# Optimization experiments

Hardware: AMD Instinct MI355X
Metric: run time of the kernel (lower is better)

The kernel has to match this reference:

```python
import jax, jax.numpy as jnp
import numpy as np

SELF_DIM = 36
ENT_DIM = 28
HID = 256


def setup_inputs() -> dict:
    key = jax.random.key(0)
    ks = jax.random.split(key, 12)
    B, agent_num, n_noisy = 32768, 20, 20
    obs_dim = SELF_DIM + ENT_DIM * (2 * agent_num - 1 + n_noisy)
    s = 0.02
    return {
        "x": jax.random.normal(ks[0], (B, obs_dim), dtype=jnp.float32),
        "Watt": jax.random.normal(ks[1], (ENT_DIM + SELF_DIM, 1), jnp.float32) * s,
        "batt": jnp.zeros((1,), jnp.float32),
        "We": jax.random.normal(ks[2], (ENT_DIM + SELF_DIM, HID), jnp.float32) * s,
        "be": jnp.zeros((HID,), jnp.float32),
        "Wse": jax.random.normal(ks[3], (2 * SELF_DIM, HID), jnp.float32) * s,
        "bse": jnp.zeros((HID,), jnp.float32),
        "Wg": jax.random.normal(ks[4], (3 * HID, 3), jnp.float32) * s,
        "bg": jnp.zeros((3,), jnp.float32),
        "Wo": jax.random.normal(ks[5], (2 * HID, HID), jnp.float32) * s,
        "bo": jnp.zeros((HID,), jnp.float32),
        "agent_num": agent_num,
    }


def reference(x, Watt, batt, We, be, Wse, bse, Wg, bg, Wo, bo, agent_num):
    B = x.shape[0]
    self_info = x[:, :SELF_DIM]  # [B,36]
    opp_end = SELF_DIM + ENT_DIM * agent_num
    par_end = opp_end + ENT_DIM * (agent_num - 1)
    opps = x[:, SELF_DIM:opp_end].reshape(B, agent_num, ENT_DIM)
    pars = x[:, opp_end:par_end].reshape(B, agent_num - 1, ENT_DIM)
    noisy = x[:, par_end:].reshape(B, -1, ENT_DIM)

    def pool(ent):
        # additive-attention pooling over one entity group
        n = ent.shape[1]
        os_ = jnp.concatenate(
            [jnp.broadcast_to(self_info[:, None, :], (B, n, SELF_DIM)), ent], axis=2
        )  # [B,n,64]
        att = jax.nn.softmax(os_ @ Watt + batt, axis=1)  # [B,n,1]
        es = os_ @ We + be  # [B,n,H]
        return jnp.sum(att * es, axis=1)  # [B,H]

    opp_e, par_e, noi_e = pool(opps), pool(pars), pool(noisy)
    group_e = jnp.stack([opp_e, par_e, noi_e], axis=1)  # [B,3,H]
    gw = jax.nn.softmax(
        jnp.concatenate([opp_e, par_e, noi_e], axis=1) @ Wg + bg, axis=1
    )  # [B,3]
    other = jnp.einsum("bg,bgh->bh", gw, group_e)  # [B,H]
    self_e = jnp.concatenate([self_info, self_info], axis=1) @ Wse + bse  # [B,H]
    obs_embedding = jnp.concatenate([other, self_e], axis=1)  # [B,2H]
    return obs_embedding @ Wo + bo
```

## Files before the change

kernel.cpp:

```cpp
#include <hip/hip_runtime.h>
#include <hip/hip_bf16.h>

#define SELF_D 36
#define ENT_D  28
#define HID    256
#define OBS    1688
#define NWAVES 8192

#define WS_A     0
#define WS_B     9216
#define WS_C     16384
#define WS_MSEL  16640
#define WS_MENT  16748
#define WS_CG    17000
#define WS_WATT  17008
#define WS_AT    17040
#define WS_BT    26256
#define WS_TOTAL 33424

__global__ __launch_bounds__(256)
void setup_kernel(const float* __restrict__ Watt, const float* __restrict__ We,
                  const float* __restrict__ be,  const float* __restrict__ Wse,
                  const float* __restrict__ bse, const float* __restrict__ Wg,
                  const float* __restrict__ bg,  const float* __restrict__ Wo,
                  const float* __restrict__ bo,  float* __restrict__ ws) {
  const int blk = blockIdx.x;
  const int c = threadIdx.x;
  if (blk < 36) {
    int k = blk;
    float acc = 0.f;
    for (int r = 0; r < 256; ++r) acc += We[k*256 + r] * Wo[r*256 + c];
    for (int r = 0; r < 256; ++r) acc += (Wse[k*256 + r] + Wse[(36+k)*256 + r]) * Wo[(256+r)*256 + c];
    ws[WS_A + k*256 + c] = acc;
    ws[WS_AT + c*36 + k] = acc;
  } else if (blk < 64) {
    int k = blk - 36;
    float acc = 0.f;
    for (int r = 0; r < 256; ++r) acc += We[(36+k)*256 + r] * Wo[r*256 + c];
    ws[WS_B + k*256 + c] = acc;
    ws[WS_BT + c*28 + k] = acc;
  } else if (blk == 64) {
    float acc = bo[c];
    for (int r = 0; r < 256; ++r) acc += be[r] * Wo[r*256 + c];
    for (int r = 0; r < 256; ++r) acc += bse[r] * Wo[(256+r)*256 + c];
    ws[WS_C + c] = acc;
  } else {
    for (int t = c; t < 391; t += 256) {
      if (t < 108) {
        int k = t / 3, j = t - 3*k;
        float acc = 0.f;
        for (int r = 0; r < 256; ++r) {
          float wg = Wg[r*3 + j] + Wg[(256+r)*3 + j] + Wg[(512+r)*3 + j];
          acc += We[k*256 + r] * wg;
        }
        ws[WS_MSEL + t] = acc;
      } else if (t < 360) {
        int idx = t - 108;
        int g = idx / 84, rem = idx - 84*g;
        int k = rem / 3, j = rem - 3*k;
        float acc = 0.f;
        for (int r = 0; r < 256; ++r) acc += We[(36+k)*256 + r] * Wg[(256*g + r)*3 + j];
        ws[WS_MENT + idx] = acc;
      } else if (t < 363) {
        int j = t - 360;
        float acc = bg[j];
        for (int r = 0; r < 256; ++r)
          acc += be[r] * (Wg[r*3 + j] + Wg[(256+r)*3 + j] + Wg[(512+r)*3 + j]);
        ws[WS_CG + j] = acc;
      } else {
        int k = t - 363;
        ws[WS_WATT + k] = Watt[36 + k];
      }
    }
  }
}

__global__ __launch_bounds__(256)
void pool_kernel(const float* __restrict__ x, const float* __restrict__ ws,
                 float* __restrict__ out, int B) {
  __shared__ __align__(16) float tile[4][OBS];
  __shared__ __align__(16) float satt[4][64];
  __shared__ __align__(16) float sebar[4][84];
  __shared__ __align__(16) float sW[28];
  __shared__ __align__(16) float sM[360];

  const int tid = threadIdx.x;
  const int w = tid >> 6, ln = tid & 63;

  for (int t = tid; t < 360; t += 256) sM[t] = ws[WS_MSEL + t];
  if (tid < 28) sW[tid] = ws[WS_WATT + tid];
  __syncthreads();

  const float cg0 = ws[WS_CG + 0], cg1 = ws[WS_CG + 1], cg2 = ws[WS_CG + 2];

  const int ent_b  = ln - (ln >= 40 ? 1 : 0);
  const bool valid = (ln < 60) && (ln != 39);
  const int ent_r  = valid ? ent_b : 0;
  int e7 = ent_r;
  while (e7 >= 7) e7 -= 7;
  const int gj = ln >> 4, gch = ln & 15;
  const bool gact = (gj < 3) && (gch < 15);

  for (int row = blockIdx.x * 4 + w; row < B; row += NWAVES) {
    const float* xr = x + (size_t)row * OBS;

#pragma unroll
    for (int i = 0; i < 7; ++i) {
      int idx = i * 64 + ln;
      if (idx < OBS / 4) {
        __builtin_amdgcn_global_load_lds(
            (const __attribute__((address_space(1))) void*)(xr + idx * 4),
            (__attribute__((address_space(3))) void*)(&tile[w][0] + idx * 4),
            16, 0, 0);
      }
    }
    asm volatile("s_waitcnt vmcnt(0)" ::: "memory");
    __builtin_amdgcn_sched_barrier(0);

    float l = -1e30f;
    {
      const float4* ep = (const float4*)&tile[w][SELF_D + ENT_D * ent_r];
      const float4* w4 = (const float4*)sW;
      float acc = 0.f;
#pragma unroll
      for (int t = 0; t < 7; ++t) {
        int c = e7 + t; if (c >= 7) c -= 7;
        float4 v = ep[c], wv = w4[c];
        acc += v.x*wv.x + v.y*wv.y + v.z*wv.z + v.w*wv.w;
      }
      if (valid) l = acc;
    }
    float m = l;
#pragma unroll
    for (int off = 32; off; off >>= 1) m = fmaxf(m, __shfl_xor(m, off));
    satt[w][ln] = valid ? __expf(l - m) : 0.f;

#pragma unroll
    for (int pass = 0; pass < 2; ++pass) {
      int t = ln + pass * 64;
      if (t < 84) {
        int g = t / 28, k = t - 28 * g;
        int e0 = g * 20 - (g >> 1);
        const float* vb = &tile[w][SELF_D + ENT_D * e0 + k];
        const float* pa = &satt[w][g * 20];
        float us = 0.f, uv = 0.f;
#pragma unroll
        for (int i = 0; i < 20; ++i) {
          float pp = pa[i];
          float vv = vb[ENT_D * i];
          us += pp; uv += pp * vv;
        }
        sebar[w][t] = uv / us;
      }
    }

    float gl = 0.f;
    if (gact) {
#pragma unroll
      for (int q = 0; q < 8; ++q) {
        int c = q * 15 + gch;
        float v = (c < SELF_D) ? tile[w][c] : sebar[w][c - SELF_D];
        gl += v * sM[c * 3 + gj];
      }
    }
#pragma unroll
    for (int off = 1; off < 16; off <<= 1) gl += __shfl_xor(gl, off);
    float l0 = __shfl(gl, 0)  + cg0;
    float l1 = __shfl(gl, 16) + cg1;
    float l2 = __shfl(gl, 32) + cg2;
    float mm = fmaxf(l0, fmaxf(l1, l2));
    float e0x = __expf(l0 - mm), e1x = __expf(l1 - mm), e2x = __expf(l2 - mm);
    float inv = 1.f / (e0x + e1x + e2x);

    float fv;
    if (ln < SELF_D) {
      fv = tile[w][ln];
    } else {
      int k = ln - SELF_D;
      fv = (e0x * sebar[w][k] + e1x * sebar[w][28 + k] + e2x * sebar[w][56 + k]) * inv;
    }
    out[(size_t)row * HID + ln] = fv;
  }
}

#define PR_ROWS 32
#define PR_CH   8
__global__ __launch_bounds__(256)
void proj_kernel(const float* __restrict__ ws, float* __restrict__ out) {
  __shared__ __align__(16) float sf[PR_CH][64];
  const int tid = threadIdx.x;

  float4 Av[9], Bv[7];
#pragma unroll
  for (int q = 0; q < 9; ++q) Av[q] = ((const float4*)(ws + WS_AT + tid * 36))[q];
#pragma unroll
  for (int q = 0; q < 7; ++q) Bv[q] = ((const float4*)(ws + WS_BT + tid * 28))[q];
  const float cc = ws[WS_C + tid];

  const size_t row0 = (size_t)blockIdx.x * PR_ROWS;
  for (int chk = 0; chk < PR_ROWS / PR_CH; ++chk) {
    const size_t rbase = row0 + chk * PR_CH;
    if (tid < PR_CH * 16) {
      int r = tid >> 4, q = tid & 15;
      ((float4*)&sf[r][0])[q] = ((const float4*)(out + (rbase + r) * HID))[q];
    }
    __syncthreads();
#pragma unroll
    for (int r = 0; r < PR_CH; ++r) {
      float acc = cc;
      const float4* f4 = (const float4*)&sf[r][0];
#pragma unroll
      for (int q = 0; q < 9; ++q) {
        float4 s = f4[q];
        acc += Av[q].x*s.x + Av[q].y*s.y + Av[q].z*s.z + Av[q].w*s.w;
      }
#pragma unroll
      for (int q = 0; q < 7; ++q) {
        float4 s = f4[9 + q];
        acc += Bv[q].x*s.x + Bv[q].y*s.y + Bv[q].z*s.z + Bv[q].w*s.w;
      }
      out[(rbase + r) * HID + tid] = acc;
    }
    __syncthreads();
  }
}

extern "C" void kernel_launch(void* const* d_in, const int* in_sizes, int n_in,
                              void* d_out, int out_size, void* d_ws, size_t ws_size,
                              hipStream_t stream) {
  const float* x    = (const float*)d_in[0];
  const float* Watt = (const float*)d_in[1];
  const float* We   = (const float*)d_in[3];
  const float* be   = (const float*)d_in[4];
  const float* Wse  = (const float*)d_in[5];
  const float* bse  = (const float*)d_in[6];
  const float* Wg   = (const float*)d_in[7];
  const float* bg   = (const float*)d_in[8];
  const float* Wo   = (const float*)d_in[9];
  const float* bo   = (const float*)d_in[10];
  float* out = (float*)d_out;
  float* ws  = (float*)d_ws;
  const int B = in_sizes[0] / OBS;

  setup_kernel<<<66, 256, 0, stream>>>(Watt, We, be, Wse, bse, Wg, bg, Wo, bo, ws);
  pool_kernel<<<NWAVES / 4, 256, 0, stream>>>(x, ws, out, B);
  proj_kernel<<<B / PR_ROWS, 256, 0, stream>>>(ws, out);
}
```

Before: 110.9 us.

## Prefetch next row into registers while computing current row in pool kernel

The pool kernel now issues global loads for the next row (row + NWAVES) into registers before computing the current row. Those values are stored into the LDS tile after compute, so memory latency overlaps with the attention math instead of stalling on a full vmcnt(0) each iteration. It also drops the rotated float4 access order in the attention dot product, which was meant to avoid LDS bank conflicts. The cost is higher register pressure from 7 float4 prefetch registers, and there may be a missing barrier between the register-to-LDS stores and the next iteration's reads, though reads are within the same wave.

```diff
diff --git a/kernel.cpp b/kernel.cpp
--- a/kernel.cpp
+++ b/kernel.cpp
@@ -96,14 +96,13 @@
   const int ent_b  = ln - (ln >= 40 ? 1 : 0);
   const bool valid = (ln < 60) && (ln != 39);
   const int ent_r  = valid ? ent_b : 0;
-  int e7 = ent_r;
-  while (e7 >= 7) e7 -= 7;
   const int gj = ln >> 4, gch = ln & 15;
   const bool gact = (gj < 3) && (gch < 15);
 
-  for (int row = blockIdx.x * 4 + w; row < B; row += NWAVES) {
-    const float* xr = x + (size_t)row * OBS;
-
+  const int row0 = blockIdx.x * 4 + w;
+
+  if (row0 < B) {
+    const float* xr = x + (size_t)row0 * OBS;
 #pragma unroll
     for (int i = 0; i < 7; ++i) {
       int idx = i * 64 + ln;
@@ -114,8 +113,26 @@
             16, 0, 0);
       }
     }
-    asm volatile("s_waitcnt vmcnt(0)" ::: "memory");
-    __builtin_amdgcn_sched_barrier(0);
+  }
+
+  for (int row = row0; row < B; row += NWAVES) {
+    const bool pfv = (row + NWAVES) < B;
+
+    float4 pf[7];
+    if (pfv) {
+      const float4* xn = (const float4*)(x + (size_t)(row + NWAVES) * OBS);
+#pragma unroll
+      for (int i = 0; i < 7; ++i) {
+        int idx = i * 64 + ln;
+        if (idx < OBS / 4) pf[i] = xn[idx];
+      }
+    }
+
+    if (row == row0) {
+      if (pfv) asm volatile("s_waitcnt vmcnt(7)" ::: "memory");
+      else     asm volatile("s_waitcnt vmcnt(0)" ::: "memory");
+      __builtin_amdgcn_sched_barrier(0);
+    }
 
     float l = -1e30f;
     {
@@ -124,8 +141,7 @@
       float acc = 0.f;
 #pragma unroll
       for (int t = 0; t < 7; ++t) {
-        int c = e7 + t; if (c >= 7) c -= 7;
-        float4 v = ep[c], wv = w4[c];
+        float4 v = ep[t], wv = w4[t];
         acc += v.x*wv.x + v.y*wv.y + v.z*wv.z + v.w*wv.w;
       }
       if (valid) l = acc;
@@ -179,6 +195,16 @@
       int k = ln - SELF_D;
       fv = (e0x * sebar[w][k] + e1x * sebar[w][28 + k] + e2x * sebar[w][56 + k]) * inv;
     }
+
+    if (pfv) {
+      float4* dst = (float4*)&tile[w][0];
+#pragma unroll
+      for (int i = 0; i < 7; ++i) {
+        int idx = i * 64 + ln;
+        if (idx < OBS / 4) dst[idx] = pf[i];
+      }
+    }
+
     out[(size_t)row * HID + ln] = fv;
   }
 }
```

Result: slower. 158.9 us (+43.3%).
